# Kernel tuning notes

Hardware: AMD Instinct MI355X
Metric: run time of the kernel (lower is better)

## Reference

```python
import jax, jax.numpy as jnp
import numpy as np

B, T, D = 1, 2048, 2048
HQ, HKV = 32, 8
DKV = 512  # HKV * head_dim

def setup_inputs() -> dict:
    key = jax.random.key(0)
    ks = jax.random.split(key, 5)
    s = 0.02
    return {
        "x": jax.random.normal(ks[0], (B, T, D), jnp.float32),
        "q_proj": jax.random.normal(ks[1], (D, D), jnp.float32) * s,
        "k_proj": jax.random.normal(ks[2], (DKV, D), jnp.float32) * s,
        "v_proj": jax.random.normal(ks[3], (DKV, D), jnp.float32) * s,
        "o_proj": jax.random.normal(ks[4], (D, D), jnp.float32) * s,
    }

def reference(x, q_proj, k_proj, v_proj, o_proj):
    b, t, _ = x.shape
    h_q, h_kv = HQ, HKV
    q_out = x @ q_proj.T            # [b,t,D]
    k_out = x @ k_proj.T            # [b,t,DKV]
    v_out = x @ v_proj.T
    dh_q = q_out.shape[-1] // h_q   # 64
    dh_k = k_out.shape[-1] // h_kv  # 64
    q = q_out.reshape(b, t, h_q, dh_q).transpose(0, 2, 1, 3)   # [b,hq,t,dh]
    k = k_out.reshape(b, t, h_kv, dh_k).transpose(0, 2, 1, 3)  # [b,hkv,t,dh]
    v = v_out.reshape(b, t, h_kv, dh_k).transpose(0, 2, 1, 3)
    group = h_q // h_kv
    k = jnp.repeat(k, group, axis=1)  # [b,hq,t,dh]
    v = jnp.repeat(v, group, axis=1)
    attn_logits = jnp.einsum('bhqd,bhkd->bhqk', q, k) / jnp.sqrt(jnp.float32(dh_q))
    mask = jnp.tril(jnp.ones((t, t), dtype=bool))
    attn = jax.nn.softmax(jnp.where(mask, attn_logits, -1e10), axis=-1)
    ctx = jnp.einsum('bhqk,bhkd->bhqd', attn, v)
    ctx = ctx.transpose(0, 2, 1, 3).reshape(b, t, o_proj.shape[0])
    return ctx @ o_proj
```

## Files before the change

kernel.cpp:

```cpp
#include <hip/hip_runtime.h>
#include <stdint.h>

typedef __attribute__((ext_vector_type(8))) __bf16 bf16x8;
typedef __attribute__((ext_vector_type(4))) float f32x4;
typedef __attribute__((ext_vector_type(4))) unsigned short u16x4;

typedef __attribute__((address_space(1))) unsigned int as1_uint;
typedef __attribute__((address_space(3))) unsigned int as3_uint;

__device__ __forceinline__ unsigned short f2bf(float f) {
  unsigned int u = __float_as_uint(f);
  u += 0x7fffu + ((u >> 16) & 1u);
  return (unsigned short)(u >> 16);
}

__device__ __forceinline__ void gload_lds16(const void* g, void* l) {
  __builtin_amdgcn_global_load_lds((as1_uint*)(uintptr_t)g, (as3_uint*)(uintptr_t)l,
                                   16, 0, 0);
}

__global__ void cvt_all(const float* __restrict__ x, const float* __restrict__ qp,
                        const float* __restrict__ kp, const float* __restrict__ vp,
                        unsigned short* __restrict__ xb, unsigned short* __restrict__ qpb,
                        unsigned short* __restrict__ kpb, unsigned short* __restrict__ vpb) {
  const int b = blockIdx.x;
  const float* in;
  unsigned short* out;
  int base;
  if (b < 4096)      { in = x;  out = xb;  base = b; }
  else if (b < 8192) { in = qp; out = qpb; base = b - 4096; }
  else if (b < 9216) { in = kp; out = kpb; base = b - 8192; }
  else               { in = vp; out = vpb; base = b - 9216; }
  const int i = base * 256 + threadIdx.x;
  float4 v = ((const float4*)in)[i];
  u16x4 o;
  o[0] = f2bf(v.x); o[1] = f2bf(v.y); o[2] = f2bf(v.z); o[3] = f2bf(v.w);
  ((u16x4*)out)[i] = o;
}

__global__ __launch_bounds__(256)
void transpose_cvt(const float* __restrict__ in, unsigned short* __restrict__ out,
                   int R, int C) {
  __shared__ unsigned short t[64][72];
  const int ti = blockIdx.y * 64;
  const int tj = blockIdx.x * 64;
  const int r  = threadIdx.x >> 4;
  const int c4 = (threadIdx.x & 15) * 4;
#pragma unroll
  for (int i = 0; i < 4; ++i) {
    int row = r + i * 16;
    float4 v = *(const float4*)&in[(size_t)(ti + row) * C + tj + c4];
    t[row][c4]     = f2bf(v.x);
    t[row][c4 + 1] = f2bf(v.y);
    t[row][c4 + 2] = f2bf(v.z);
    t[row][c4 + 3] = f2bf(v.w);
  }
  __syncthreads();
#pragma unroll
  for (int i = 0; i < 4; ++i) {
    int orow = r + i * 16;
    u16x4 o;
    o[0] = t[c4][orow]; o[1] = t[c4 + 1][orow];
    o[2] = t[c4 + 2][orow]; o[3] = t[c4 + 3][orow];
    *(u16x4*)&out[(size_t)(tj + orow) * R + ti + c4] = o;
  }
}

template <int BN, bool OUT_BF16>
__device__ __forceinline__
void gemm_body(const unsigned short* __restrict__ A,
               const unsigned short* __restrict__ B,
               void* __restrict__ Cout, int N, int K, float alpha,
               int bx, int by, unsigned short* lA, unsigned short* lB) {
  constexpr int NF  = BN / 32;
  constexpr int ASZ = 64 * 64;
  constexpr int BSZ = BN * 64;
  const int tid  = threadIdx.x;
  const int lane = tid & 63;
  const int w    = tid >> 6;
  const int wr   = (w >> 1) * 32;
  const int wc   = (w & 1) * (BN / 2);
  const long brow = (long)by * 64;
  const long bcol = (long)bx * BN;
  const int lr = lane & 15;
  const int lq = lane >> 4;

  const int row0 = tid >> 3;
  const int lc0  = (tid & 7) ^ (row0 & 7);

  f32x4 acc[2][NF] = {};

  const unsigned short* gA = A + (brow + row0) * (long)K + lc0 * 8;
  const unsigned short* gB = B + (bcol + row0) * (long)K + lc0 * 8;

#define G_STAGE(buf, k0)                                                          \
  {                                                                               \
    gload_lds16(gA + (k0),           lA + (buf) * ASZ + tid * 8);                 \
    gload_lds16(gA + 32l * K + (k0), lA + (buf) * ASZ + 2048 + tid * 8);          \
    _Pragma("unroll")                                                             \
    for (int g = 0; g < NF; ++g)                                                  \
      gload_lds16(gB + g * 32l * K + (k0), lB + (buf) * BSZ + g * 2048 + tid * 8);\
  }

  G_STAGE(0, 0);
  __syncthreads();

  for (int k0 = 0; k0 < K; k0 += 64) {
    const int cur = (k0 >> 6) & 1;
    if (k0 + 64 < K) G_STAGE(cur ^ 1, k0 + 64);
#pragma unroll
    for (int kk = 0; kk < 2; ++kk) {
      const int j = kk * 4 + lq;
      const int ra0 = wr + lr, ra1 = wr + 16 + lr;
      bf16x8 a0 = *(const bf16x8*)&lA[cur * ASZ + ra0 * 64 + ((j ^ (ra0 & 7)) << 3)];
      bf16x8 a1 = *(const bf16x8*)&lA[cur * ASZ + ra1 * 64 + ((j ^ (ra1 & 7)) << 3)];
      bf16x8 b[NF];
#pragma unroll
      for (int n = 0; n < NF; ++n) {
        const int rb = wc + n * 16 + lr;
        b[n] = *(const bf16x8*)&lB[cur * BSZ + rb * 64 + ((j ^ (rb & 7)) << 3)];
      }
#pragma unroll
      for (int n = 0; n < NF; ++n) {
        acc[0][n] = __builtin_amdgcn_mfma_f32_16x16x32_bf16(a0, b[n], acc[0][n], 0, 0, 0);
        acc[1][n] = __builtin_amdgcn_mfma_f32_16x16x32_bf16(a1, b[n], acc[1][n], 0, 0, 0);
      }
    }
    __syncthreads();
  }
#undef G_STAGE

  const int orow = (int)brow + wr + lq * 4;
  const int ocol = (int)bcol + wc + lr;
#pragma unroll
  for (int m = 0; m < 2; ++m)
#pragma unroll
    for (int n = 0; n < NF; ++n)
#pragma unroll
      for (int r = 0; r < 4; ++r) {
        size_t row = (size_t)(orow + m * 16 + r);
        size_t col = (size_t)(ocol + n * 16);
        float v = acc[m][n][r] * alpha;
        if (OUT_BF16)
          ((unsigned short*)Cout)[row * N + col] = f2bf(v);
        else
          ((float*)Cout)[row * N + col] = v;
      }
}

template <int BN, bool OUT_BF16>
__global__ __launch_bounds__(256)
void gemm_nt(const unsigned short* __restrict__ A,
             const unsigned short* __restrict__ B,
             void* __restrict__ Cout, int N, int K, float alpha) {
  __shared__ unsigned short lA[2 * 64 * 64];
  __shared__ unsigned short lB[2 * BN * 64];
  gemm_body<BN, OUT_BF16>(A, B, Cout, N, K, alpha, blockIdx.x, blockIdx.y, lA, lB);
}

__global__ __launch_bounds__(256)
void gemm_proj(const unsigned short* __restrict__ xb,
               const unsigned short* __restrict__ qpb,
               const unsigned short* __restrict__ kpb,
               const unsigned short* __restrict__ vpb,
               unsigned short* __restrict__ Qb, unsigned short* __restrict__ Kbf,
               unsigned short* __restrict__ Vtb) {
  __shared__ unsigned short lA[2 * 64 * 64];
  __shared__ unsigned short lB[2 * 128 * 64];
  const int bid = blockIdx.x;
  const unsigned short *A, *B;
  unsigned short* C;
  int N, bx, by;
  float alpha;
  if (bid < 512) {
    A = xb;  B = qpb; C = Qb;  N = 2048; alpha = 0.125f * 1.44269504088896f;
    bx = bid & 15; by = bid >> 4;
  } else if (bid < 640) {
    int b = bid - 512;
    A = xb;  B = kpb; C = Kbf; N = 512;  alpha = 1.0f;
    bx = b & 3; by = b >> 2;
  } else {
    int b = bid - 640;
    A = vpb; B = xb;  C = Vtb; N = 2048; alpha = 1.0f;
    bx = b & 15; by = b >> 4;
  }
  gemm_body<128, true>(A, B, C, N, 2048, alpha, bx, by, lA, lB);
}

__global__ __launch_bounds__(256, 4)
void attn64(const unsigned short* __restrict__ Q,
            const unsigned short* __restrict__ Kb,
            const unsigned short* __restrict__ Vt,
            unsigned short* __restrict__ ctx) {
  constexpr int T = 2048, DQ = 2048, DKV = 512, DH = 64;
  const int h    = blockIdx.x;
  const int hkv  = h >> 2;
  const int ya   = blockIdx.y >> 3;
  const int yb   = blockIdx.y & 7;
  const int qi   = (ya == 0) ? yb : (ya == 1) ? 15 - yb : (ya == 2) ? 16 + yb : 31 - yb;
  const int tid  = threadIdx.x;
  const int lane = tid & 63;
  const int w    = tid >> 6;
  const int lr   = lane & 15;
  const int lq   = lane >> 4;
  const int lk   = lq * 8;
  const int sw   = lr & 7;

  __shared__ unsigned short lK[2][64 * 64];
  __shared__ unsigned short lV[2][64 * 64];
  __shared__ unsigned short P[4][16][64];

  const int row0 = tid >> 3;
  const int lc0  = (tid & 7) ^ (row0 & 7);

  bf16x8 ones_frag;
#pragma unroll
  for (int i = 0; i < 8; ++i) ones_frag[i] = (lr == 0) ? (__bf16)1.0f : (__bf16)0.0f;

#define STAGE_KV(bufidx, kv0)                                                        \
  {                                                                                  \
    gload_lds16(Kb + (size_t)((kv0) + row0) * DKV + hkv * DH + lc0 * 8,              \
                &lK[bufidx][tid * 8]);                                               \
    gload_lds16(Kb + (size_t)((kv0) + row0 + 32) * DKV + hkv * DH + lc0 * 8,         \
                &lK[bufidx][2048 + tid * 8]);                                        \
    gload_lds16(Vt + (size_t)(hkv * DH + row0) * T + (kv0) + lc0 * 8,                \
                &lV[bufidx][tid * 8]);                                               \
    gload_lds16(Vt + (size_t)(hkv * DH + row0 + 32) * T + (kv0) + lc0 * 8,           \
                &lV[bufidx][2048 + tid * 8]);                                        \
  }

  const int q0b = qi * 64;
  const int qw  = q0b + w * 16;

  bf16x8 qf0 = *(const bf16x8*)&Q[(size_t)(qw + lr) * DQ + h * DH + lk];
  bf16x8 qf1 = *(const bf16x8*)&Q[(size_t)(qw + lr) * DQ + h * DH + 32 + lk];

  f32x4 oacc[4] = {};
  f32x4 lacc = {};
  float mr[4];
#pragma unroll
  for (int r = 0; r < 4; ++r) mr[r] = -3.0e38f;

  const int nt = qi + 1;
  STAGE_KV(0, 0);
  __syncthreads();

  for (int t = 0; t < nt; ++t) {
    const int kv0 = t * 64;
    const int cur = t & 1;
    if (t + 1 < nt) STAGE_KV(cur ^ 1, kv0 + 64);

    f32x4 s[4];
    __builtin_amdgcn_s_setprio(1);
#pragma unroll
    for (int n = 0; n < 4; ++n) {
      const int krow = n * 16 + lr;
      bf16x8 kf0 = *(const bf16x8*)&lK[cur][krow * 64 + ((lq ^ sw) << 3)];
      bf16x8 kf1 = *(const bf16x8*)&lK[cur][krow * 64 + (((4 + lq) ^ sw) << 3)];
      f32x4 acc = {};
      acc = __builtin_amdgcn_mfma_f32_16x16x32_bf16(qf0, kf0, acc, 0, 0, 0);
      acc = __builtin_amdgcn_mfma_f32_16x16x32_bf16(qf1, kf1, acc, 0, 0, 0);
      s[n] = acc;
    }
    __builtin_amdgcn_s_setprio(0);

    if (t == qi) {
      const int qr0 = qw + (lq << 2);
#pragma unroll
      for (int n = 0; n < 4; ++n) {
        int kc = kv0 + n * 16 + lr;
#pragma unroll
        for (int r = 0; r < 4; ++r)
          if (kc > qr0 + r) s[n][r] = -3.0e38f;
      }
    }

    float lml[4];
#pragma unroll
    for (int r = 0; r < 4; ++r)
      lml[r] = fmaxf(fmaxf(s[0][r], s[1][r]), fmaxf(s[2][r], s[3][r]));
    const bool defer = __all((lml[0] <= mr[0] + 8.f) & (lml[1] <= mr[1] + 8.f) &
                             (lml[2] <= mr[2] + 8.f) & (lml[3] <= mr[3] + 8.f));
    if (!defer) {
#pragma unroll
      for (int r = 0; r < 4; ++r) {
        float ml = lml[r];
        ml = fmaxf(ml, __shfl_xor(ml, 1));
        ml = fmaxf(ml, __shfl_xor(ml, 2));
        ml = fmaxf(ml, __shfl_xor(ml, 4));
        ml = fmaxf(ml, __shfl_xor(ml, 8));
        float mnew = fmaxf(mr[r], ml);
        float sc   = __builtin_amdgcn_exp2f(mr[r] - mnew);
        mr[r] = mnew;
        lacc[r] *= sc;
        oacc[0][r] *= sc; oacc[1][r] *= sc;
        oacc[2][r] *= sc; oacc[3][r] *= sc;
      }
    }

#pragma unroll
    for (int n = 0; n < 4; ++n)
#pragma unroll
      for (int r = 0; r < 4; ++r)
        s[n][r] = __builtin_amdgcn_exp2f(s[n][r] - mr[r]);

#pragma unroll
    for (int n = 0; n < 4; ++n)
#pragma unroll
      for (int r = 0; r < 4; ++r) {
        const int prow = (lq << 2) + r;
        P[w][prow][(((2 * n + (lr >> 3)) ^ (prow & 7)) << 3) + (lr & 7)] =
            (unsigned short)(__float_as_uint(s[n][r]) >> 16);
      }
    asm volatile("s_waitcnt lgkmcnt(0)" ::: "memory");
    __builtin_amdgcn_sched_barrier(0);

    __builtin_amdgcn_s_setprio(1);
#pragma unroll
    for (int ks = 0; ks < 2; ++ks) {
      bf16x8 pf = *(const bf16x8*)&P[w][lr][((ks * 4 + lq) ^ sw) << 3];
      lacc = __builtin_amdgcn_mfma_f32_16x16x32_bf16(pf, ones_frag, lacc, 0, 0, 0);
#pragma unroll
      for (int n = 0; n < 4; ++n) {
        const int vrow = n * 16 + lr;
        bf16x8 vf = *(const bf16x8*)&lV[cur][vrow * 64 + (((ks * 4 + lq) ^ sw) << 3)];
        oacc[n] = __builtin_amdgcn_mfma_f32_16x16x32_bf16(pf, vf, oacc[n], 0, 0, 0);
      }
    }
    __builtin_amdgcn_s_setprio(0);

    __syncthreads();
  }

  float inv[4];
#pragma unroll
  for (int r = 0; r < 4; ++r) {
    float l = __shfl(lacc[r], lane & 48);
    inv[r] = 1.f / l;
  }
#pragma unroll
  for (int n = 0; n < 4; ++n)
#pragma unroll
    for (int r = 0; r < 4; ++r) {
      int qrow = qw + (lq << 2) + r;
      ctx[(size_t)qrow * DQ + h * DH + n * 16 + lr] = f2bf(oacc[n][r] * inv[r]);
    }
#undef STAGE_KV
}

extern "C" void kernel_launch(void* const* d_in, const int* in_sizes, int n_in,
                              void* d_out, int out_size, void* d_ws, size_t ws_size,
                              hipStream_t stream) {
  const float* x  = (const float*)d_in[0];
  const float* qp = (const float*)d_in[1];
  const float* kp = (const float*)d_in[2];
  const float* vp = (const float*)d_in[3];
  const float* op = (const float*)d_in[4];

  char* ws = (char*)d_ws;
  const size_t MB = 1024 * 1024;
  unsigned short* xb   = (unsigned short*)(ws + 0 * MB);
  unsigned short* qpb  = (unsigned short*)(ws + 8 * MB);
  unsigned short* kpb  = (unsigned short*)(ws + 16 * MB);
  unsigned short* vpb  = (unsigned short*)(ws + 18 * MB);
  unsigned short* opT  = (unsigned short*)(ws + 20 * MB);
  unsigned short* Qb   = (unsigned short*)(ws + 28 * MB);
  unsigned short* Kbf  = (unsigned short*)(ws + 36 * MB);
  unsigned short* Vtb  = (unsigned short*)(ws + 38 * MB);
  unsigned short* ctxb = (unsigned short*)(ws + 40 * MB);

  cvt_all<<<10240, 256, 0, stream>>>(x, qp, kp, vp, xb, qpb, kpb, vpb);
  transpose_cvt<<<dim3(32, 32), 256, 0, stream>>>(op, opT, 2048, 2048);

  gemm_proj<<<768, 256, 0, stream>>>(xb, qpb, kpb, vpb, Qb, Kbf, Vtb);

  attn64<<<dim3(32, 32), 256, 0, stream>>>(Qb, Kbf, Vtb, ctxb);

  gemm_nt<128, false><<<dim3(16, 32), 256, 0, stream>>>(ctxb, opT, d_out, 2048, 2048, 1.0f);
}
```

Baseline: 113.8 us.

## Use two waves per attention block with 32 query rows each; fuse conversion kernels

The attention kernel now runs 128 threads (2 waves) per block, and each wave handles two 16-row query tiles. Each K fragment loaded from LDS is reused across two MFMA row tiles, and the K/V staging loop is rewritten for the smaller thread count. Separately, the bf16 conversion and the transpose-convert of the output projection are merged into one launch to save a kernel launch. The change trades higher register pressure per wave and fewer waves per block for better LDS reuse.

Result: slower. 124.1 us (+9.0%).

```diff
diff --git a/kernel.cpp b/kernel.cpp
--- a/kernel.cpp
+++ b/kernel.cpp
@@ -19,37 +19,39 @@
                                    16, 0, 0);
 }
 
-__global__ void cvt_all(const float* __restrict__ x, const float* __restrict__ qp,
-                        const float* __restrict__ kp, const float* __restrict__ vp,
-                        unsigned short* __restrict__ xb, unsigned short* __restrict__ qpb,
-                        unsigned short* __restrict__ kpb, unsigned short* __restrict__ vpb) {
+__global__ __launch_bounds__(256)
+void cvt_fused(const float* __restrict__ x, const float* __restrict__ qp,
+               const float* __restrict__ kp, const float* __restrict__ vp,
+               const float* __restrict__ op,
+               unsigned short* __restrict__ xb, unsigned short* __restrict__ qpb,
+               unsigned short* __restrict__ kpb, unsigned short* __restrict__ vpb,
+               unsigned short* __restrict__ opT) {
+  __shared__ unsigned short t[64][72];
   const int b = blockIdx.x;
-  const float* in;
-  unsigned short* out;
-  int base;
-  if (b < 4096)      { in = x;  out = xb;  base = b; }
-  else if (b < 8192) { in = qp; out = qpb; base = b - 4096; }
-  else if (b < 9216) { in = kp; out = kpb; base = b - 8192; }
-  else               { in = vp; out = vpb; base = b - 9216; }
-  const int i = base * 256 + threadIdx.x;
-  float4 v = ((const float4*)in)[i];
-  u16x4 o;
-  o[0] = f2bf(v.x); o[1] = f2bf(v.y); o[2] = f2bf(v.z); o[3] = f2bf(v.w);
-  ((u16x4*)out)[i] = o;
-}
-
-__global__ __launch_bounds__(256)
-void transpose_cvt(const float* __restrict__ in, unsigned short* __restrict__ out,
-                   int R, int C) {
-  __shared__ unsigned short t[64][72];
-  const int ti = blockIdx.y * 64;
-  const int tj = blockIdx.x * 64;
+  if (b < 10240) {
+    const float* in;
+    unsigned short* out;
+    int base;
+    if (b < 4096)      { in = x;  out = xb;  base = b; }
+    else if (b < 8192) { in = qp; out = qpb; base = b - 4096; }
+    else if (b < 9216) { in = kp; out = kpb; base = b - 8192; }
+    else               { in = vp; out = vpb; base = b - 9216; }
+    const int i = base * 256 + threadIdx.x;
+    float4 v = ((const float4*)in)[i];
+    u16x4 o;
+    o[0] = f2bf(v.x); o[1] = f2bf(v.y); o[2] = f2bf(v.z); o[3] = f2bf(v.w);
+    ((u16x4*)out)[i] = o;
+    return;
+  }
+  const int tb = b - 10240;
+  const int tj = (tb & 31) * 64;
+  const int ti = (tb >> 5) * 64;
   const int r  = threadIdx.x >> 4;
   const int c4 = (threadIdx.x & 15) * 4;
 #pragma unroll
   for (int i = 0; i < 4; ++i) {
     int row = r + i * 16;
-    float4 v = *(const float4*)&in[(size_t)(ti + row) * C + tj + c4];
+    float4 v = *(const float4*)&op[(size_t)(ti + row) * 2048 + tj + c4];
     t[row][c4]     = f2bf(v.x);
     t[row][c4 + 1] = f2bf(v.y);
     t[row][c4 + 2] = f2bf(v.z);
@@ -62,7 +64,7 @@
     u16x4 o;
     o[0] = t[c4][orow]; o[1] = t[c4 + 1][orow];
     o[2] = t[c4 + 2][orow]; o[3] = t[c4 + 3][orow];
-    *(u16x4*)&out[(size_t)(tj + orow) * R + ti + c4] = o;
+    *(u16x4*)&opT[(size_t)(tj + orow) * 2048 + ti + c4] = o;
   }
 }
 
@@ -187,7 +189,7 @@
   gemm_body<128, true>(A, B, C, N, 2048, alpha, bx, by, lA, lB);
 }
 
-__global__ __launch_bounds__(256, 4)
+__global__ __launch_bounds__(128, 2)
 void attn64(const unsigned short* __restrict__ Q,
             const unsigned short* __restrict__ Kb,
             const unsigned short* __restrict__ Vt,
@@ -200,7 +202,7 @@
   const int qi   = (ya == 0) ? yb : (ya == 1) ? 15 - yb : (ya == 2) ? 16 + yb : 31 - yb;
   const int tid  = threadIdx.x;
   const int lane = tid & 63;
-  const int w    = tid >> 6;
+  const int wv   = tid >> 6;
   const int lr   = lane & 15;
   const int lq   = lane >> 4;
   const int lk   = lq * 8;
@@ -208,7 +210,7 @@
 
   __shared__ unsigned short lK[2][64 * 64];
   __shared__ unsigned short lV[2][64 * 64];
-  __shared__ unsigned short P[4][16][64];
+  __shared__ unsigned short P[2][32][64];
 
   const int row0 = tid >> 3;
   const int lc0  = (tid & 7) ^ (row0 & 7);
@@ -219,27 +221,33 @@
 
 #define STAGE_KV(bufidx, kv0)                                                        \
   {                                                                                  \
-    gload_lds16(Kb + (size_t)((kv0) + row0) * DKV + hkv * DH + lc0 * 8,              \
-                &lK[bufidx][tid * 8]);                                               \
-    gload_lds16(Kb + (size_t)((kv0) + row0 + 32) * DKV + hkv * DH + lc0 * 8,         \
-                &lK[bufidx][2048 + tid * 8]);                                        \
-    gload_lds16(Vt + (size_t)(hkv * DH + row0) * T + (kv0) + lc0 * 8,                \
-                &lV[bufidx][tid * 8]);                                               \
-    gload_lds16(Vt + (size_t)(hkv * DH + row0 + 32) * T + (kv0) + lc0 * 8,           \
-                &lV[bufidx][2048 + tid * 8]);                                        \
+    _Pragma("unroll")                                                                \
+    for (int g = 0; g < 4; ++g)                                                      \
+      gload_lds16(Kb + (size_t)((kv0) + row0 + 16 * g) * DKV + hkv * DH + lc0 * 8,   \
+                  &lK[bufidx][tid * 8 + g * 1024]);                                  \
+    _Pragma("unroll")                                                                \
+    for (int g = 0; g < 4; ++g)                                                      \
+      gload_lds16(Vt + (size_t)(hkv * DH + row0 + 16 * g) * T + (kv0) + lc0 * 8,     \
+                  &lV[bufidx][tid * 8 + g * 1024]);                                  \
   }
 
   const int q0b = qi * 64;
-  const int qw  = q0b + w * 16;
-
-  bf16x8 qf0 = *(const bf16x8*)&Q[(size_t)(qw + lr) * DQ + h * DH + lk];
-  bf16x8 qf1 = *(const bf16x8*)&Q[(size_t)(qw + lr) * DQ + h * DH + 32 + lk];
-
-  f32x4 oacc[4] = {};
-  f32x4 lacc = {};
-  float mr[4];
-#pragma unroll
-  for (int r = 0; r < 4; ++r) mr[r] = -3.0e38f;
+  const int qwv = q0b + 32 * wv;
+
+  bf16x8 qf[2][2];
+#pragma unroll
+  for (int rt = 0; rt < 2; ++rt) {
+    qf[rt][0] = *(const bf16x8*)&Q[(size_t)(qwv + 16 * rt + lr) * DQ + h * DH + lk];
+    qf[rt][1] = *(const bf16x8*)&Q[(size_t)(qwv + 16 * rt + lr) * DQ + h * DH + 32 + lk];
+  }
+
+  f32x4 oacc[2][4] = {};
+  f32x4 lacc[2] = {};
+  float mr[2][4];
+#pragma unroll
+  for (int rt = 0; rt < 2; ++rt)
+#pragma unroll
+    for (int r = 0; r < 4; ++r) mr[rt][r] = -3.0e38f;
 
   const int nt = qi + 1;
   STAGE_KV(0, 0);
@@ -250,81 +258,95 @@
     const int cur = t & 1;
     if (t + 1 < nt) STAGE_KV(cur ^ 1, kv0 + 64);
 
-    f32x4 s[4];
+    f32x4 s[2][4];
     __builtin_amdgcn_s_setprio(1);
 #pragma unroll
     for (int n = 0; n < 4; ++n) {
       const int krow = n * 16 + lr;
       bf16x8 kf0 = *(const bf16x8*)&lK[cur][krow * 64 + ((lq ^ sw) << 3)];
       bf16x8 kf1 = *(const bf16x8*)&lK[cur][krow * 64 + (((4 + lq) ^ sw) << 3)];
-      f32x4 acc = {};
-      acc = __builtin_amdgcn_mfma_f32_16x16x32_bf16(qf0, kf0, acc, 0, 0, 0);
-      acc = __builtin_amdgcn_mfma_f32_16x16x32_bf16(qf1, kf1, acc, 0, 0, 0);
-      s[n] = acc;
+#pragma unroll
+      for (int rt = 0; rt < 2; ++rt) {
+        f32x4 acc = {};
+        acc = __builtin_amdgcn_mfma_f32_16x16x32_bf16(qf[rt][0], kf0, acc, 0, 0, 0);
+        acc = __builtin_amdgcn_mfma_f32_16x16x32_bf16(qf[rt][1], kf1, acc, 0, 0, 0);
+        s[rt][n] = acc;
+      }
     }
     __builtin_amdgcn_s_setprio(0);
 
     if (t == qi) {
-      const int qr0 = qw + (lq << 2);
-#pragma unroll
-      for (int n = 0; n < 4; ++n) {
-        int kc = kv0 + n * 16 + lr;
-#pragma unroll
-        for (int r = 0; r < 4; ++r)
-          if (kc > qr0 + r) s[n][r] = -3.0e38f;
-      }
-    }
-
-    float lml[4];
-#pragma unroll
-    for (int r = 0; r < 4; ++r)
-      lml[r] = fmaxf(fmaxf(s[0][r], s[1][r]), fmaxf(s[2][r], s[3][r]));
-    const bool defer = __all((lml[0] <= mr[0] + 8.f) & (lml[1] <= mr[1] + 8.f) &
-                             (lml[2] <= mr[2] + 8.f) & (lml[3] <= mr[3] + 8.f));
+#pragma unroll
+      for (int rt = 0; rt < 2; ++rt) {
+        const int qr0 = qwv + 16 * rt + (lq << 2);
+#pragma unroll
+        for (int n = 0; n < 4; ++n) {
+          int kc = kv0 + n * 16 + lr;
+#pragma unroll
+          for (int r = 0; r < 4; ++r)
+            if (kc > qr0 + r) s[rt][n][r] = -3.0e38f;
+        }
+      }
+    }
+
+    float lml[2][4];
+#pragma unroll
+    for (int rt = 0; rt < 2; ++rt)
+#pragma unroll
+      for (int r = 0; r < 4; ++r)
+        lml[rt][r] = fmaxf(fmaxf(s[rt][0][r], s[rt][1][r]),
+                           fmaxf(s[rt][2][r], s[rt][3][r]));
+    const bool defer = __all(
+        (lml[0][0] <= mr[0][0] + 8.f) & (lml[0][1] <= mr[0][1] + 8.f) &
+        (lml[0][2] <= mr[0][2] + 8.f) & (lml[0][3] <= mr[0][3] + 8.f) &
+        (lml[1][0] <= mr[1][0] + 8.f) & (lml[1][1] <= mr[1][1] + 8.f) &
+        (lml[1][2] <= mr[1][2] + 8.f) & (lml[1][3] <= mr[1][3] + 8.f));
     if (!defer) {
 #pragma unroll
-      for (int r = 0; r < 4; ++r) {
-        float ml = lml[r];
-        ml = fmaxf(ml, __shfl_xor(ml, 1));
-        ml = fmaxf(ml, __shfl_xor(ml, 2));
-        ml = fmaxf(ml, __shfl_xor(ml, 4));
-        ml = fmaxf(ml, __shfl_xor(ml, 8));
-        float mnew = fmaxf(mr[r], ml);
-        float sc   = __builtin_amdgcn_exp2f(mr[r] - mnew);
-        mr[r] = mnew;
-        lacc[r] *= sc;
-        oacc[0][r] *= sc; oacc[1][r] *= sc;
-        oacc[2][r] *= sc; oacc[3][r] *= sc;
-      }
-    }
-
-#pragma unroll
-    for (int n = 0; n < 4; ++n)
-#pragma unroll
-      for (int r = 0; r < 4; ++r)
-        s[n][r] = __builtin_amdgcn_exp2f(s[n][r] - mr[r]);
-
-#pragma unroll
-    for (int n = 0; n < 4; ++n)
-#pragma unroll
-      for (int r = 0; r < 4; ++r) {
-        const int prow = (lq << 2) + r;
-        P[w][prow][(((2 * n + (lr >> 3)) ^ (prow & 7)) << 3) + (lr & 7)] =
-            (unsigned short)(__float_as_uint(s[n][r]) >> 16);
-      }
+      for (int rt = 0; rt < 2; ++rt)
+#pragma unroll
+        for (int r = 0; r < 4; ++r) {
+          float ml = lml[rt][r];
+          ml = fmaxf(ml, __shfl_xor(ml, 1));
+          ml = fmaxf(ml, __shfl_xor(ml, 2));
+          ml = fmaxf(ml, __shfl_xor(ml, 4));
+          ml = fmaxf(ml, __shfl_xor(ml, 8));
+          float mnew = fmaxf(mr[rt][r], ml);
+          float sc   = __builtin_amdgcn_exp2f(mr[rt][r] - mnew);
+          mr[rt][r] = mnew;
+          lacc[rt][r] *= sc;
+          oacc[rt][0][r] *= sc; oacc[rt][1][r] *= sc;
+          oacc[rt][2][r] *= sc; oacc[rt][3][r] *= sc;
+        }
+    }
+
+#pragma unroll
+    for (int rt = 0; rt < 2; ++rt)
+#pragma unroll
+      for (int n = 0; n < 4; ++n)
+#pragma unroll
+        for (int r = 0; r < 4; ++r) {
+          float p = __builtin_amdgcn_exp2f(s[rt][n][r] - mr[rt][r]);
+          const int prow = 16 * rt + (lq << 2) + r;
+          P[wv][prow][(((2 * n + (lr >> 3)) ^ (prow & 7)) << 3) + (lr & 7)] =
+              (unsigned short)(__float_as_uint(p) >> 16);
+        }
     asm volatile("s_waitcnt lgkmcnt(0)" ::: "memory");
     __builtin_amdgcn_sched_barrier(0);
 
     __builtin_amdgcn_s_setprio(1);
 #pragma unroll
     for (int ks = 0; ks < 2; ++ks) {
-      bf16x8 pf = *(const bf16x8*)&P[w][lr][((ks * 4 + lq) ^ sw) << 3];
-      lacc = __builtin_amdgcn_mfma_f32_16x16x32_bf16(pf, ones_frag, lacc, 0, 0, 0);
+      bf16x8 pf0 = *(const bf16x8*)&P[wv][lr][((ks * 4 + lq) ^ sw) << 3];
+      bf16x8 pf1 = *(const bf16x8*)&P[wv][16 + lr][((ks * 4 + lq) ^ sw) << 3];
+      lacc[0] = __builtin_amdgcn_mfma_f32_16x16x32_bf16(pf0, ones_frag, lacc[0], 0, 0, 0);
+      lacc[1] = __builtin_amdgcn_mfma_f32_16x16x32_bf16(pf1, ones_frag, lacc[1], 0, 0, 0);
 #pragma unroll
       for (int n = 0; n < 4; ++n) {
         const int vrow = n * 16 + lr;
         bf16x8 vf = *(const bf16x8*)&lV[cur][vrow * 64 + (((ks * 4 + lq) ^ sw) << 3)];
-        oacc[n] = __builtin_amdgcn_mfma_f32_16x16x32_bf16(pf, vf, oacc[n], 0, 0, 0);
+        oacc[0][n] = __builtin_amdgcn_mfma_f32_16x16x32_bf16(pf0, vf, oacc[0][n], 0, 0, 0);
+        oacc[1][n] = __builtin_amdgcn_mfma_f32_16x16x32_bf16(pf1, vf, oacc[1][n], 0, 0, 0);
       }
     }
     __builtin_amdgcn_s_setprio(0);
@@ -332,19 +354,22 @@
     __syncthreads();
   }
 
-  float inv[4];
-#pragma unroll
-  for (int r = 0; r < 4; ++r) {
-    float l = __shfl(lacc[r], lane & 48);
-    inv[r] = 1.f / l;
-  }
-#pragma unroll
-  for (int n = 0; n < 4; ++n)
+#pragma unroll
+  for (int rt = 0; rt < 2; ++rt) {
+    float inv[4];
 #pragma unroll
     for (int r = 0; r < 4; ++r) {
-      int qrow = qw + (lq << 2) + r;
-      ctx[(size_t)qrow * DQ + h * DH + n * 16 + lr] = f2bf(oacc[n][r] * inv[r]);
-    }
+      float l = __shfl(lacc[rt][r], lane & 48);
+      inv[r] = 1.f / l;
+    }
+#pragma unroll
+    for (int n = 0; n < 4; ++n)
+#pragma unroll
+      for (int r = 0; r < 4; ++r) {
+        int qrow = qwv + 16 * rt + (lq << 2) + r;
+        ctx[(size_t)qrow * DQ + h * DH + n * 16 + lr] = f2bf(oacc[rt][n][r] * inv[r]);
+      }
+  }
 #undef STAGE_KV
 }
 
@@ -369,12 +394,11 @@
   unsigned short* Vtb  = (unsigned short*)(ws + 38 * MB);
   unsigned short* ctxb = (unsigned short*)(ws + 40 * MB);
 
-  cvt_all<<<10240, 256, 0, stream>>>(x, qp, kp, vp, xb, qpb, kpb, vpb);
-  transpose_cvt<<<dim3(32, 32), 256, 0, stream>>>(op, opT, 2048, 2048);
+  cvt_fused<<<11264, 256, 0, stream>>>(x, qp, kp, vp, op, xb, qpb, kpb, vpb, opT);
 
   gemm_proj<<<768, 256, 0, stream>>>(xb, qpb, kpb, vpb, Qb, Kbf, Vtb);
 
-  attn64<<<dim3(32, 32), 256, 0, stream>>>(Qb, Kbf, Vtb, ctxb);
+  attn64<<<dim3(32, 32), 128, 0, stream>>>(Qb, Kbf, Vtb, ctxb);
 
   gemm_nt<128, false><<<dim3(16, 32), 256, 0, stream>>>(ctxb, opT, d_out, 2048, 2048, 1.0f);
 }
```
